# Kernel tuning notes

Hardware: AMD Instinct MI355X
Metric: run time of the kernel (lower is better)

Reference implementation:

```python
import jax, jax.numpy as jnp
import numpy as np

GROUPS = 8


def setup_inputs() -> dict:
    key = jax.random.key(0)
    k1, k2, k3 = jax.random.split(key, 3)
    B, H, W, Cin, Cout, KH, KW = 32, 56, 56, 256, 256, 3, 3
    inputs = jax.random.normal(k1, (B, H, W, Cin), dtype=jnp.float32)
    # HWIO kernel for grouped conv: input channel dim = Cin // groups
    fan_in = KH * KW * (Cin // GROUPS)
    limit = np.sqrt(6.0 / (fan_in + Cout // GROUPS))  # glorot-ish scale
    kernel = jax.random.uniform(k2, (KH, KW, Cin // GROUPS, Cout), dtype=jnp.float32,
                                minval=-limit, maxval=limit)
    bias = jnp.zeros((Cout,), dtype=jnp.float32)
    return {"inputs": inputs, "kernel": kernel, "bias": bias}


def reference(inputs, kernel, bias):
    # Equivalent to per-group slice + Conv2D + concat: a single grouped conv.
    # inputs: [B,H,W,Cin] NHWC; kernel: [KH,KW,Cin//G,Cout] HWIO
    out = jax.lax.conv_general_dilated(
        inputs, kernel,
        window_strides=(1, 1),
        padding="SAME",
        lhs_dilation=(1, 1),
        rhs_dilation=(1, 1),
        dimension_numbers=("NHWC", "HWIO", "NHWC"),
        feature_group_count=GROUPS,
    )
    out = out + bias  # broadcast over [B,H,W,Cout]
    return out
```

## Files before the change

kernel.cpp:

```cpp
#include <hip/hip_runtime.h>


#define R_ 4

typedef __bf16 bf16x8 __attribute__((ext_vector_type(8)));
typedef float floatx4 __attribute__((ext_vector_type(4)));
typedef unsigned short ushortx4 __attribute__((ext_vector_type(4)));
typedef unsigned short ushortx8 __attribute__((ext_vector_type(8)));

#define IMG_USHORTS 25690112u
#define WGT_USHORTS 73728u
#define ZPAD_USHORTS 64u

__device__ __forceinline__ unsigned short f2bf(float f) {
    unsigned int u = __builtin_bit_cast(unsigned int, f);
    u += 0x7fffu + ((u >> 16) & 1u);
    return (unsigned short)(u >> 16);
}

__global__ __launch_bounds__(256)
void iprep(const float* __restrict__ in, unsigned short* __restrict__ obf) {
    const int n8 = 3211264;
    const int stride = gridDim.x * 256;
    for (int i = blockIdx.x * 256 + threadIdx.x; i < n8; i += stride) {
        const float4 a = *reinterpret_cast<const float4*>(&in[i * 8]);
        const float4 b = *reinterpret_cast<const float4*>(&in[i * 8 + 4]);
        ushortx8 p;
        p[0] = f2bf(a.x); p[1] = f2bf(a.y); p[2] = f2bf(a.z); p[3] = f2bf(a.w);
        p[4] = f2bf(b.x); p[5] = f2bf(b.y); p[6] = f2bf(b.z); p[7] = f2bf(b.w);
        *reinterpret_cast<ushortx8*>(&obf[i * 8]) = p;
    }
}

__global__ __launch_bounds__(256)
void wprep(const float* __restrict__ wgt, unsigned short* __restrict__ wbf) {
    const int i = blockIdx.x * 256 + threadIdx.x;
    if (blockIdx.x == 0 && threadIdx.x < ZPAD_USHORTS)
        wbf[WGT_USHORTS + threadIdx.x] = 0;
    const int co256 = i & 255;
    const int tmp   = i >> 8;
    const int ci    = tmp & 31;
    const int kk    = tmp >> 5;
    const int g  = co256 >> 5;
    const int co = co256 & 31;
    wbf[((g * 9 + kk) * 32 + co) * 32 + ci] = f2bf(wgt[i]);
}

__global__ __launch_bounds__(256, 7)
void gconv_bf16(const unsigned short* __restrict__ bfin,
                const unsigned short* __restrict__ wbf,
                const float* __restrict__ bias, float* __restrict__ out) {
    const int rt = blockIdx.x;
    const int g  = blockIdx.y;
    const int b  = blockIdx.z;
    const int y0 = rt * R_;

    __shared__ unsigned short lds_in[352 * 32];

    const int tid  = threadIdx.x;
    const int wv   = tid >> 6;
    const int lane = tid & 63;
    const unsigned short* zpad = wbf + WGT_USHORTS;

    for (int i = wv; i < 22; i += 4) {
        const int s   = (i << 4) + (lane >> 2);
        const int row = s / 58;
        const int col = s - row * 58;
        const unsigned gy = (unsigned)(y0 - 1 + row);
        const unsigned gx = (unsigned)(col - 1);
        const bool ok = (s < 348) & (gy < 56u) & (gx < 56u);
        const unsigned short* src = ok
            ? &bfin[(((b * 56 + (int)gy) * 56 + (int)gx) << 8) + (g << 5) + ((lane & 3) << 3)]
            : zpad;
        __builtin_amdgcn_global_load_lds(
            (const __attribute__((address_space(1))) void*)src,
            (__attribute__((address_space(3))) void*)&lds_in[i << 9],
            16, 0, 0);
    }

    __syncthreads();

    const int lc   = lane & 15;
    const int quad = lane >> 4;

    const int nt = (wv < 2) ? 4 : 3;
    const int t0 = (wv < 2) ? (wv * 4) : (8 + (wv - 2) * 3);

    int lane_base[4];
#pragma unroll
    for (int t = 0; t < 4; ++t) {
        const int tt = (t < nt) ? (t0 + t) : 0;
        const int p  = tt * 16 + lc;
        const int yl = p / 56;
        lane_base[t] = (yl * 58 + (p - yl * 56)) * 32 + (quad << 3);
    }

    const unsigned short* wq = &wbf[(g * 9 * 32) * 32 + (quad << 3)];

    floatx4 acc[4][2];
#pragma unroll
    for (int t = 0; t < 4; ++t) { acc[t][0] = (floatx4)(0.f); acc[t][1] = (floatx4)(0.f); }

    bf16x8 b0 = *reinterpret_cast<const bf16x8*>(&wq[(0 * 32 + lc) * 32]);
    bf16x8 b1 = *reinterpret_cast<const bf16x8*>(&wq[(0 * 32 + 16 + lc) * 32]);

#pragma unroll
    for (int kk = 0; kk < 9; ++kk) {
        const int koff = ((kk / 3) * 58 + (kk % 3)) * 32;
        bf16x8 nb0 = b0, nb1 = b1;
        if (kk < 8) {
            nb0 = *reinterpret_cast<const bf16x8*>(&wq[((kk + 1) * 32 + lc) * 32]);
            nb1 = *reinterpret_cast<const bf16x8*>(&wq[((kk + 1) * 32 + 16 + lc) * 32]);
        }
#pragma unroll
        for (int t = 0; t < 4; ++t) {
            if (t < nt) {
                const bf16x8 a = *reinterpret_cast<const bf16x8*>(
                    &lds_in[lane_base[t] + koff]);
                acc[t][0] = __builtin_amdgcn_mfma_f32_16x16x32_bf16(b0, a, acc[t][0], 0, 0, 0);
                acc[t][1] = __builtin_amdgcn_mfma_f32_16x16x32_bf16(b1, a, acc[t][1], 0, 0, 0);
            }
        }
        b0 = nb0; b1 = nb1;
    }

    const float4 bv0 = *reinterpret_cast<const float4*>(&bias[(g << 5) + (quad << 2)]);
    const float4 bv1 = *reinterpret_cast<const float4*>(&bias[(g << 5) + 16 + (quad << 2)]);
    const int obase = (((b * 56 + y0) * 56) << 8) + (g << 5) + (quad << 2);
#pragma unroll
    for (int t = 0; t < 4; ++t) {
        if (t < nt) {
            const int p = (t0 + t) * 16 + lc;
            const int y = p / 56;
            const int x = p - y * 56;
            float* o = &out[obase + ((y * 56 + x) << 8)];
            float4 s0, s1;
            s0.x = acc[t][0][0] + bv0.x; s0.y = acc[t][0][1] + bv0.y;
            s0.z = acc[t][0][2] + bv0.z; s0.w = acc[t][0][3] + bv0.w;
            s1.x = acc[t][1][0] + bv1.x; s1.y = acc[t][1][1] + bv1.y;
            s1.z = acc[t][1][2] + bv1.z; s1.w = acc[t][1][3] + bv1.w;
            *reinterpret_cast<float4*>(o)      = s0;
            *reinterpret_cast<float4*>(o + 16) = s1;
        }
    }
}

__global__ __launch_bounds__(256, 7)
void gconv_f32s(const float* __restrict__ in, const unsigned short* __restrict__ wbf,
                const float* __restrict__ bias, float* __restrict__ out) {
    const int rt = blockIdx.x, g = blockIdx.y, b = blockIdx.z;
    const int y0 = rt * R_;
    __shared__ unsigned short lds_in[6 * 58 * 32];
    const int tid = threadIdx.x;
#pragma unroll
    for (int i = 0; i < 11; ++i) {
        const int c = tid + (i << 8);
        if (c < 6 * 58 * 8) {
            const int row = c / 464, rem = c - row * 464, col = rem >> 3, q = rem & 7;
            const int gy = y0 - 1 + row, gx = col - 1;
            float4 v = make_float4(0.f, 0.f, 0.f, 0.f);
            if ((unsigned)gy < 56u && (unsigned)gx < 56u)
                v = *reinterpret_cast<const float4*>(
                    &in[((((b * 56 + gy) * 56 + gx)) << 8) + (g << 5) + (q << 2)]);
            ushortx4 p;
            p.x = f2bf(v.x); p.y = f2bf(v.y); p.z = f2bf(v.z); p.w = f2bf(v.w);
            *reinterpret_cast<ushortx4*>(&lds_in[(row * 58 + col) * 32 + (q << 2)]) = p;
        }
    }
    __syncthreads();
    const int wv = tid >> 6, lane = tid & 63, lc = lane & 15, quad = lane >> 4;
    const int nt = (wv < 2) ? 4 : 3;
    const int t0 = (wv < 2) ? (wv * 4) : (8 + (wv - 2) * 3);
    int lane_base[4];
#pragma unroll
    for (int t = 0; t < 4; ++t) {
        const int tt = (t < nt) ? (t0 + t) : 0;
        const int p = tt * 16 + lc;
        const int yl = p / 56;
        lane_base[t] = (yl * 58 + (p - yl * 56)) * 32 + (quad << 3);
    }
    const unsigned short* wq = &wbf[(g * 9 * 32) * 32 + (quad << 3)];
    floatx4 acc[4][2];
#pragma unroll
    for (int t = 0; t < 4; ++t) { acc[t][0] = (floatx4)(0.f); acc[t][1] = (floatx4)(0.f); }
    bf16x8 b0 = *reinterpret_cast<const bf16x8*>(&wq[(0 * 32 + lc) * 32]);
    bf16x8 b1 = *reinterpret_cast<const bf16x8*>(&wq[(0 * 32 + 16 + lc) * 32]);
#pragma unroll
    for (int kk = 0; kk < 9; ++kk) {
        const int koff = ((kk / 3) * 58 + (kk % 3)) * 32;
        bf16x8 nb0 = b0, nb1 = b1;
        if (kk < 8) {
            nb0 = *reinterpret_cast<const bf16x8*>(&wq[((kk + 1) * 32 + lc) * 32]);
            nb1 = *reinterpret_cast<const bf16x8*>(&wq[((kk + 1) * 32 + 16 + lc) * 32]);
        }
#pragma unroll
        for (int t = 0; t < 4; ++t) {
            if (t < nt) {
                const bf16x8 a = *reinterpret_cast<const bf16x8*>(&lds_in[lane_base[t] + koff]);
                acc[t][0] = __builtin_amdgcn_mfma_f32_16x16x32_bf16(b0, a, acc[t][0], 0, 0, 0);
                acc[t][1] = __builtin_amdgcn_mfma_f32_16x16x32_bf16(b1, a, acc[t][1], 0, 0, 0);
            }
        }
        b0 = nb0; b1 = nb1;
    }
    const float4 bv0 = *reinterpret_cast<const float4*>(&bias[(g << 5) + (quad << 2)]);
    const float4 bv1 = *reinterpret_cast<const float4*>(&bias[(g << 5) + 16 + (quad << 2)]);
    const int obase = (((b * 56 + y0) * 56) << 8) + (g << 5) + (quad << 2);
#pragma unroll
    for (int t = 0; t < 4; ++t) {
        if (t < nt) {
            const int p = (t0 + t) * 16 + lc;
            const int y = p / 56, x = p - y * 56;
            float* o = &out[obase + ((y * 56 + x) << 8)];
            float4 s0, s1;
            s0.x = acc[t][0][0] + bv0.x; s0.y = acc[t][0][1] + bv0.y;
            s0.z = acc[t][0][2] + bv0.z; s0.w = acc[t][0][3] + bv0.w;
            s1.x = acc[t][1][0] + bv1.x; s1.y = acc[t][1][1] + bv1.y;
            s1.z = acc[t][1][2] + bv1.z; s1.w = acc[t][1][3] + bv1.w;
            *reinterpret_cast<float4*>(o)      = s0;
            *reinterpret_cast<float4*>(o + 16) = s1;
        }
    }
}

__global__ __launch_bounds__(256, 2)
void gconv_mfma_ldsw(const float* __restrict__ in, const float* __restrict__ wgt,
                     const float* __restrict__ bias, float* __restrict__ out) {
    const int rt = blockIdx.x, g = blockIdx.y, b = blockIdx.z;
    const int y0 = rt * 8;
    __shared__ unsigned short lds_in[10 * 58 * 32];
    __shared__ unsigned short lds_w[9 * 32 * 32];
    const int tid = threadIdx.x;
    for (int i = tid; i < 9 * 32 * 32; i += 256) {
        const int co = i & 31, ci = (i >> 5) & 31, kk = i >> 10;
        lds_w[(kk * 32 + co) * 32 + ci] = f2bf(wgt[(kk * 32 + ci) * 256 + g * 32 + co]);
    }
    for (int c = tid; c < 10 * 58 * 8; c += 256) {
        const int row = c / 464, rem = c - row * 464, col = rem >> 3, q = rem & 7;
        const int gy = y0 - 1 + row, gx = col - 1;
        float4 v = make_float4(0.f, 0.f, 0.f, 0.f);
        if ((unsigned)gy < 56u && (unsigned)gx < 56u)
            v = *reinterpret_cast<const float4*>(&in[(((b * 56 + gy) * 56 + gx) * 256) + g * 32 + q * 4]);
        ushortx4 p;
        p.x = f2bf(v.x); p.y = f2bf(v.y); p.z = f2bf(v.z); p.w = f2bf(v.w);
        *reinterpret_cast<ushortx4*>(&lds_in[(row * 58 + col) * 32 + q * 4]) = p;
    }
    __syncthreads();
    const int wv = tid >> 6, lane = tid & 63, lc = lane & 15, quad = lane >> 4;
    int lane_base[7];
#pragma unroll
    for (int t = 0; t < 7; ++t) {
        const int p = (wv * 7 + t) * 16 + lc;
        const int yl = p / 56, xl = p - yl * 56;
        lane_base[t] = (yl * 58 + xl) * 32 + quad * 8;
    }
    floatx4 acc[7][2];
#pragma unroll
    for (int t = 0; t < 7; ++t) { acc[t][0] = (floatx4)(0.f); acc[t][1] = (floatx4)(0.f); }
#pragma unroll
    for (int kk = 0; kk < 9; ++kk) {
        const int ky = kk / 3, kx = kk % 3;
        const int koff = (ky * 58 + kx) * 32;
        const bf16x8 bf0 = *reinterpret_cast<const bf16x8*>(&lds_w[(kk * 32 + lc) * 32 + quad * 8]);
        const bf16x8 bf1 = *reinterpret_cast<const bf16x8*>(&lds_w[(kk * 32 + 16 + lc) * 32 + quad * 8]);
#pragma unroll
        for (int t = 0; t < 7; ++t) {
            const bf16x8 a = *reinterpret_cast<const bf16x8*>(&lds_in[lane_base[t] + koff]);
            acc[t][0] = __builtin_amdgcn_mfma_f32_16x16x32_bf16(a, bf0, acc[t][0], 0, 0, 0);
            acc[t][1] = __builtin_amdgcn_mfma_f32_16x16x32_bf16(a, bf1, acc[t][1], 0, 0, 0);
        }
    }
    const float bv0 = bias[g * 32 + lc], bv1 = bias[g * 32 + 16 + lc];
#pragma unroll
    for (int t = 0; t < 7; ++t)
#pragma unroll
        for (int r = 0; r < 4; ++r) {
            const int p = (wv * 7 + t) * 16 + quad * 4 + r;
            const int y = p / 56, x = p - y * 56;
            float* o = &out[(((b * 56) + y0 + y) * 56 + x) * 256 + g * 32];
            o[lc] = acc[t][0][r] + bv0;
            o[16 + lc] = acc[t][1][r] + bv1;
        }
}

extern "C" void kernel_launch(void* const* d_in, const int* in_sizes, int n_in,
                              void* d_out, int out_size, void* d_ws, size_t ws_size,
                              hipStream_t stream) {
    const float* in   = (const float*)d_in[0];
    const float* wgt  = (const float*)d_in[1];
    const float* bias = (const float*)d_in[2];
    float* out        = (float*)d_out;

    const size_t need_full = (size_t)(IMG_USHORTS + WGT_USHORTS + ZPAD_USHORTS) * 2;
    const size_t need_wgt  = (size_t)WGT_USHORTS * 2;

    if (d_ws != nullptr && ws_size >= need_full) {
        unsigned short* bfin = (unsigned short*)d_ws;
        unsigned short* wbf  = bfin + IMG_USHORTS;
        iprep<<<dim3(2048, 1, 1), dim3(256, 1, 1), 0, stream>>>(in, bfin);
        wprep<<<dim3(288, 1, 1), dim3(256, 1, 1), 0, stream>>>(wgt, wbf);
        gconv_bf16<<<dim3(14, 8, 32), dim3(256, 1, 1), 0, stream>>>(bfin, wbf, bias, out);
    } else if (d_ws != nullptr && ws_size >= need_wgt) {
        unsigned short* wbf = (unsigned short*)d_ws;
        wprep<<<dim3(288, 1, 1), dim3(256, 1, 1), 0, stream>>>(wgt, wbf);
        gconv_f32s<<<dim3(14, 8, 32), dim3(256, 1, 1), 0, stream>>>(in, wbf, bias, out);
    } else {
        gconv_mfma_ldsw<<<dim3(7, 8, 32), dim3(256, 1, 1), 0, stream>>>(in, wgt, bias, out);
    }
}
```

Baseline: 225.4 us.

## Pre-pad bf16 image in workspace and read MFMA operands directly from global

The input prep kernel now writes a zero-padded 58x58 bf16 image, so the conv kernel no longer needs boundary checks. The conv kernel drops its LDS staging and barrier and loads each MFMA A-operand straight from global memory, relying on L1/L2 caching for the 3x3 reuse. The occupancy hint drops from 7 to 4 waves. The cost is a larger prep pass and nine uncoalesced-ish global loads per tile instead of LDS reads.

```diff
diff --git a/kernel.cpp b/kernel.cpp
--- a/kernel.cpp
+++ b/kernel.cpp
@@ -8,9 +8,9 @@
 typedef unsigned short ushortx4 __attribute__((ext_vector_type(4)));
 typedef unsigned short ushortx8 __attribute__((ext_vector_type(8)));
 
-#define IMG_USHORTS 25690112u
 #define WGT_USHORTS 73728u
-#define ZPAD_USHORTS 64u
+#define WGT_PAD     73792u
+#define PIMG_USHORTS 27557888u
 
 __device__ __forceinline__ unsigned short f2bf(float f) {
     unsigned int u = __builtin_bit_cast(unsigned int, f);
@@ -19,24 +19,8 @@
 }
 
 __global__ __launch_bounds__(256)
-void iprep(const float* __restrict__ in, unsigned short* __restrict__ obf) {
-    const int n8 = 3211264;
-    const int stride = gridDim.x * 256;
-    for (int i = blockIdx.x * 256 + threadIdx.x; i < n8; i += stride) {
-        const float4 a = *reinterpret_cast<const float4*>(&in[i * 8]);
-        const float4 b = *reinterpret_cast<const float4*>(&in[i * 8 + 4]);
-        ushortx8 p;
-        p[0] = f2bf(a.x); p[1] = f2bf(a.y); p[2] = f2bf(a.z); p[3] = f2bf(a.w);
-        p[4] = f2bf(b.x); p[5] = f2bf(b.y); p[6] = f2bf(b.z); p[7] = f2bf(b.w);
-        *reinterpret_cast<ushortx8*>(&obf[i * 8]) = p;
-    }
-}
-
-__global__ __launch_bounds__(256)
 void wprep(const float* __restrict__ wgt, unsigned short* __restrict__ wbf) {
     const int i = blockIdx.x * 256 + threadIdx.x;
-    if (blockIdx.x == 0 && threadIdx.x < ZPAD_USHORTS)
-        wbf[WGT_USHORTS + threadIdx.x] = 0;
     const int co256 = i & 255;
     const int tmp   = i >> 8;
     const int ci    = tmp & 31;
@@ -46,53 +30,56 @@
     wbf[((g * 9 + kk) * 32 + co) * 32 + ci] = f2bf(wgt[i]);
 }
 
-__global__ __launch_bounds__(256, 7)
-void gconv_bf16(const unsigned short* __restrict__ bfin,
-                const unsigned short* __restrict__ wbf,
-                const float* __restrict__ bias, float* __restrict__ out) {
+__global__ __launch_bounds__(256)
+void iprep_pad(const float* __restrict__ in, unsigned short* __restrict__ pimg) {
+    const int n8 = 3444736;
+    const int stride = gridDim.x * 256;
+    for (int i = blockIdx.x * 256 + threadIdx.x; i < n8; i += stride) {
+        const int c8 = i & 31;
+        const int s  = i >> 5;
+        const int x  = s % 58;
+        const int t  = s / 58;
+        const int y  = t % 58;
+        const int b  = t / 58;
+        ushortx8 p = (ushortx8)(0);
+        if (y >= 1 && y <= 56 && x >= 1 && x <= 56) {
+            const float* q = &in[((((b * 56 + (y - 1)) * 56) + (x - 1)) << 8) + (c8 << 3)];
+            const float4 a  = *reinterpret_cast<const float4*>(q);
+            const float4 b4 = *reinterpret_cast<const float4*>(q + 4);
+            p[0] = f2bf(a.x);  p[1] = f2bf(a.y);  p[2] = f2bf(a.z);  p[3] = f2bf(a.w);
+            p[4] = f2bf(b4.x); p[5] = f2bf(b4.y); p[6] = f2bf(b4.z); p[7] = f2bf(b4.w);
+        }
+        *reinterpret_cast<ushortx8*>(&pimg[i * 8]) = p;
+    }
+}
+
+__global__ __launch_bounds__(256, 4)
+void gconv_direct(const unsigned short* __restrict__ pimg,
+                  const unsigned short* __restrict__ wbf,
+                  const float* __restrict__ bias, float* __restrict__ out) {
     const int rt = blockIdx.x;
     const int g  = blockIdx.y;
     const int b  = blockIdx.z;
     const int y0 = rt * R_;
 
-    __shared__ unsigned short lds_in[352 * 32];
-
     const int tid  = threadIdx.x;
     const int wv   = tid >> 6;
     const int lane = tid & 63;
-    const unsigned short* zpad = wbf + WGT_USHORTS;
-
-    for (int i = wv; i < 22; i += 4) {
-        const int s   = (i << 4) + (lane >> 2);
-        const int row = s / 58;
-        const int col = s - row * 58;
-        const unsigned gy = (unsigned)(y0 - 1 + row);
-        const unsigned gx = (unsigned)(col - 1);
-        const bool ok = (s < 348) & (gy < 56u) & (gx < 56u);
-        const unsigned short* src = ok
-            ? &bfin[(((b * 56 + (int)gy) * 56 + (int)gx) << 8) + (g << 5) + ((lane & 3) << 3)]
-            : zpad;
-        __builtin_amdgcn_global_load_lds(
-            (const __attribute__((address_space(1))) void*)src,
-            (__attribute__((address_space(3))) void*)&lds_in[i << 9],
-            16, 0, 0);
-    }
-
-    __syncthreads();
-
     const int lc   = lane & 15;
     const int quad = lane >> 4;
 
     const int nt = (wv < 2) ? 4 : 3;
     const int t0 = (wv < 2) ? (wv * 4) : (8 + (wv - 2) * 3);
 
-    int lane_base[4];
+    int pbase[4];
 #pragma unroll
     for (int t = 0; t < 4; ++t) {
         const int tt = (t < nt) ? (t0 + t) : 0;
         const int p  = tt * 16 + lc;
         const int yl = p / 56;
-        lane_base[t] = (yl * 58 + (p - yl * 56)) * 32 + (quad << 3);
+        const int xl = p - yl * 56;
+        const int slice = b * 3364 + (y0 + yl) * 58 + xl;
+        pbase[t] = (slice << 8) + (g << 5) + (quad << 3);
     }
 
     const unsigned short* wq = &wbf[(g * 9 * 32) * 32 + (quad << 3)];
@@ -106,7 +93,7 @@
 
 #pragma unroll
     for (int kk = 0; kk < 9; ++kk) {
-        const int koff = ((kk / 3) * 58 + (kk % 3)) * 32;
+        const int koff = ((kk / 3) * 58 + (kk % 3)) << 8;
         bf16x8 nb0 = b0, nb1 = b1;
         if (kk < 8) {
             nb0 = *reinterpret_cast<const bf16x8*>(&wq[((kk + 1) * 32 + lc) * 32]);
@@ -115,8 +102,7 @@
 #pragma unroll
         for (int t = 0; t < 4; ++t) {
             if (t < nt) {
-                const bf16x8 a = *reinterpret_cast<const bf16x8*>(
-                    &lds_in[lane_base[t] + koff]);
+                const bf16x8 a = *reinterpret_cast<const bf16x8*>(&pimg[pbase[t] + koff]);
                 acc[t][0] = __builtin_amdgcn_mfma_f32_16x16x32_bf16(b0, a, acc[t][0], 0, 0, 0);
                 acc[t][1] = __builtin_amdgcn_mfma_f32_16x16x32_bf16(b1, a, acc[t][1], 0, 0, 0);
             }
@@ -291,15 +277,15 @@
     const float* bias = (const float*)d_in[2];
     float* out        = (float*)d_out;
 
-    const size_t need_full = (size_t)(IMG_USHORTS + WGT_USHORTS + ZPAD_USHORTS) * 2;
+    const size_t need_full = (size_t)(WGT_PAD + PIMG_USHORTS) * 2;
     const size_t need_wgt  = (size_t)WGT_USHORTS * 2;
 
     if (d_ws != nullptr && ws_size >= need_full) {
-        unsigned short* bfin = (unsigned short*)d_ws;
-        unsigned short* wbf  = bfin + IMG_USHORTS;
-        iprep<<<dim3(2048, 1, 1), dim3(256, 1, 1), 0, stream>>>(in, bfin);
+        unsigned short* wbf  = (unsigned short*)d_ws;
+        unsigned short* pimg = wbf + WGT_PAD;
         wprep<<<dim3(288, 1, 1), dim3(256, 1, 1), 0, stream>>>(wgt, wbf);
-        gconv_bf16<<<dim3(14, 8, 32), dim3(256, 1, 1), 0, stream>>>(bfin, wbf, bias, out);
+        iprep_pad<<<dim3(2048, 1, 1), dim3(256, 1, 1), 0, stream>>>(in, pimg);
+        gconv_direct<<<dim3(14, 8, 32), dim3(256, 1, 1), 0, stream>>>(pimg, wbf, bias, out);
     } else if (d_ws != nullptr && ws_size >= need_wgt) {
         unsigned short* wbf = (unsigned short*)d_ws;
         wprep<<<dim3(288, 1, 1), dim3(256, 1, 1), 0, stream>>>(wgt, wbf);
```

New measurement: 267.3 us. 1.19x slower.
